# Kernel tuning notes

Measured on AMD Instinct MI355X. Metric: run time of the kernel, lower is better.

## Reference

```python
import jax, jax.numpy as jnp
import numpy as np

PATCH = 8          # patch_size
KEEP_RATIO = 0.7   # keep_ratio at full pruning progress (epoch >= 2*warmup)
MIN_PATCHES = 10


def setup_inputs() -> dict:
    key = jax.random.key(0)
    k_t, k_w1, k_w2 = jax.random.split(key, 3)
    B, H, W, C = 16, 128, 128, 256
    hidden = C // 4
    tokens = jax.random.normal(k_t, (B, H * W, C), dtype=jnp.float32)
    W1 = jax.random.normal(k_w1, (C, hidden), dtype=jnp.float32) * (1.0 / np.sqrt(C))
    b1 = jnp.zeros((hidden,), dtype=jnp.float32)
    W2 = jax.random.normal(k_w2, (hidden, 1), dtype=jnp.float32) * (1.0 / np.sqrt(hidden))
    b2 = jnp.zeros((1,), dtype=jnp.float32)
    return {"tokens": tokens, "W1": W1, "b1": b1, "W2": W2, "b2": b2, "H": H, "W": W}


def reference(tokens, W1, b1, W2, b2, H, W):
    B, N, C = tokens.shape
    ph = pw = PATCH
    nh, nw = H // ph, W // pw              # patches per dim (H,W divisible by PATCH)
    nP = nh * nw

    # ---- unfold into patches: [B, nP, ph*pw, C] (matches torch unfold layout) ----
    x = tokens.reshape(B, nh, ph, nw, pw, C)
    patches_flat = x.transpose(0, 1, 3, 2, 4, 5).reshape(B, nP, ph * pw, C)

    # ---- per-token importance (learnable MLP scorer), mean over patch tokens ----
    h = jax.nn.relu(jnp.einsum('bptc,cd->bptd', patches_flat, W1) + b1)
    tok_imp = jax.nn.sigmoid(jnp.einsum('bptd,do->bpto', h, W2) + b2)[..., 0]  # [B,nP,ph*pw]
    scores = tok_imp.mean(axis=-1)                                             # [B,nP]

    # ---- top-k patch selection, sorted ascending (keeps spatial order) ----
    nK = max(MIN_PATCHES, int(nP * KEEP_RATIO))  # 179 for 256 patches
    _, top_idx = jax.lax.top_k(scores, nK)
    top_idx = jnp.sort(top_idx, axis=-1)         # [B,nK]

    # ---- gather kept patches: [B, nK, ph, pw, C] ----
    patches = patches_flat.reshape(B, nP, ph, pw, C)
    kept = jnp.take_along_axis(patches, top_idx[:, :, None, None, None], axis=1)

    # ---- pad with zero patches to a full nKh x nKw grid, re-assemble 2D map ----
    nKh = -(-nK // nw)            # ceil
    nKw = min(nK, nw)
    pad = nKh * nKw - nK
    kept = jnp.pad(kept, ((0, 0), (0, pad), (0, 0), (0, 0), (0, 0)))
    out2d = kept.reshape(B, nKh, nKw, ph, pw, C).transpose(0, 1, 3, 2, 4, 5)
    H_new, W_new = nKh * ph, nKw * pw
    pruned_tokens = out2d.reshape(B, H_new * W_new, C)
    return pruned_tokens
```

## Files before the change

### kernel.cpp

```cpp
#include <hip/hip_runtime.h>
#include <math.h>

#define CCH   256
#define HID   64
#define MT    256
#define KC    32
#define XT    258
#define NP    256
#define NK    179
#define NSLOT 192
#define IMW   128
#define OUTH  96

typedef float f32x4 __attribute__((ext_vector_type(4)));

__global__ __launch_bounds__(256) void scorer_kernel(
    const float* __restrict__ tokens, const float* __restrict__ W1,
    const float* __restrict__ b1, const float* __restrict__ W2,
    const float* __restrict__ b2v, float* __restrict__ tok_imp)
{
    __shared__ float xs[KC * XT];
    __shared__ float ws[KC * HID];
    __shared__ float red[8 * MT];

    const int t  = threadIdx.x;
    const int tw = t & 31;
    const int hg = t >> 5;
    const long base = (long)blockIdx.x * MT;

    float w2r[8];
    float acc[8][8];
    #pragma unroll
    for (int j = 0; j < 8; ++j) w2r[j] = W2[hg * 8 + j];
    {
        float binit[8];
        #pragma unroll
        for (int j = 0; j < 8; ++j) binit[j] = b1[hg * 8 + j];
        #pragma unroll
        for (int i = 0; i < 8; ++i)
            #pragma unroll
            for (int j = 0; j < 8; ++j) acc[i][j] = binit[j];
    }

    const float4* tok4 = (const float4*)(tokens + base * CCH);
    const int f4k = t & 7;
    const int tl0 = t >> 3;

    float4 pf[8];
    #pragma unroll
    for (int pass = 0; pass < 8; ++pass)
        pf[pass] = tok4[(long)(tl0 + 32 * pass) * (CCH / 4) + f4k];
    float4 wpf0 = ((const float4*)W1)[t];
    float4 wpf1 = ((const float4*)W1)[t + 256];

    for (int ch = 0; ch < CCH / KC; ++ch) {
        #pragma unroll
        for (int pass = 0; pass < 8; ++pass) {
            int tokLocal = tl0 + 32 * pass;
            float4 v = pf[pass];
            int kloc = f4k * 4;
            xs[(kloc + 0) * XT + tokLocal] = v.x;
            xs[(kloc + 1) * XT + tokLocal] = v.y;
            xs[(kloc + 2) * XT + tokLocal] = v.z;
            xs[(kloc + 3) * XT + tokLocal] = v.w;
        }
        ((float4*)ws)[t]       = wpf0;
        ((float4*)ws)[t + 256] = wpf1;
        __syncthreads();

        if (ch < CCH / KC - 1) {
            #pragma unroll
            for (int pass = 0; pass < 8; ++pass)
                pf[pass] = tok4[(long)(tl0 + 32 * pass) * (CCH / 4)
                                + (ch + 1) * (KC / 4) + f4k];
            const float4* w14 = (const float4*)(W1 + (ch + 1) * KC * HID);
            wpf0 = w14[t];
            wpf1 = w14[t + 256];
        }

        #pragma unroll
        for (int kk = 0; kk < KC; ++kk) {
            float xv[8], wv[8];
            #pragma unroll
            for (int g = 0; g < 4; ++g) {
                xv[2 * g]     = xs[kk * XT + g * 64 + 2 * tw];
                xv[2 * g + 1] = xs[kk * XT + g * 64 + 2 * tw + 1];
            }
            #pragma unroll
            for (int j = 0; j < 8; ++j) wv[j] = ws[kk * HID + hg * 8 + j];
            #pragma unroll
            for (int i = 0; i < 8; ++i)
                #pragma unroll
                for (int j = 0; j < 8; ++j)
                    acc[i][j] = fmaf(xv[i], wv[j], acc[i][j]);
        }
        __syncthreads();
    }

    #pragma unroll
    for (int i = 0; i < 8; ++i) {
        float p = 0.f;
        #pragma unroll
        for (int j = 0; j < 8; ++j) {
            float h = acc[i][j] > 0.f ? acc[i][j] : 0.f;
            p = fmaf(h, w2r[j], p);
        }
        int g  = i >> 1;
        int lt = g * 64 + 2 * tw + (i & 1);
        red[hg * MT + lt] = p;
    }
    __syncthreads();
    float s = b2v[0];
    #pragma unroll
    for (int g = 0; g < 8; ++g) s += red[g * MT + t];
    tok_imp[base + t] = 1.f / (1.f + expf(-s));
}

__global__ __launch_bounds__(256) void select_kernel(
    const float* __restrict__ tok_imp, int* __restrict__ sel)
{
    __shared__ float s[NP];
    __shared__ unsigned long long wmask[4];
    const int b = blockIdx.x, p = threadIdx.x;
    const int ih = p >> 4, iw = p & 15;
    const float4* tp4 = (const float4*)(tok_imp + (long)b * 16384
                                        + (ih * 8) * IMW + iw * 8);
    float sum = 0.f;
    #pragma unroll
    for (int ti = 0; ti < 8; ++ti) {
        float4 a = tp4[ti * (IMW / 4)];
        float4 c = tp4[ti * (IMW / 4) + 1];
        sum += a.x; sum += a.y; sum += a.z; sum += a.w;
        sum += c.x; sum += c.y; sum += c.z; sum += c.w;
    }
    s[p] = sum;
    __syncthreads();
    const float sp = s[p];
    int rank = 0;
    #pragma unroll 8
    for (int j = 0; j < NP; ++j) {
        float sj = s[j];
        rank += (sj > sp) || ((sj == sp) && (j < p));
    }
    const bool keep = rank < NK;
    const unsigned long long m = __ballot(keep);
    const int wv = p >> 6, ln = p & 63;
    if (ln == 0) wmask[wv] = m;
    __syncthreads();
    if (keep) {
        int pos = __popcll(m & ((1ull << ln) - 1ull));
        #pragma unroll
        for (int w = 0; w < 3; ++w)
            if (w < wv) pos += __popcll(wmask[w]);
        sel[b * NK + pos] = p;
    }
}

__global__ __launch_bounds__(256) void gather_kernel(
    const float* __restrict__ tokens, const int* __restrict__ sel,
    float* __restrict__ out)
{
    const int bid = blockIdx.x;
    const int b = bid / NSLOT, k = bid % NSLOT;
    const int t = threadIdx.x;
    const int kh = k >> 4, kw = k & 15;
    f32x4* dst4 = (f32x4*)(out + (long)b * OUTH * IMW * CCH);

    if (k >= NK) {
        const f32x4 z = {0.f, 0.f, 0.f, 0.f};
        #pragma unroll
        for (int i = 0; i < 16; ++i) {
            int f = i * 256 + t;
            int ti = f >> 9;
            int off = f & 511;
            long d = ((long)(kh * 8 + ti) * IMW + kw * 8) * (CCH / 4) + off;
            __builtin_nontemporal_store(z, &dst4[d]);
        }
        return;
    }
    const int p = sel[b * NK + k];
    const int ih = p >> 4, iw = p & 15;
    const f32x4* src4 = (const f32x4*)(tokens + (long)b * 16384 * CCH);
    #pragma unroll
    for (int i = 0; i < 16; ++i) {
        int f = i * 256 + t;
        int ti = f >> 9;
        int off = f & 511;
        long srow = ((long)(ih * 8 + ti) * IMW + iw * 8) * (CCH / 4) + off;
        long drow = ((long)(kh * 8 + ti) * IMW + kw * 8) * (CCH / 4) + off;
        f32x4 v = src4[srow];
        __builtin_nontemporal_store(v, &dst4[drow]);
    }
}

extern "C" void kernel_launch(void* const* d_in, const int* in_sizes, int n_in,
                              void* d_out, int out_size, void* d_ws, size_t ws_size,
                              hipStream_t stream)
{
    const float* tokens = (const float*)d_in[0];
    const float* W1     = (const float*)d_in[1];
    const float* b1     = (const float*)d_in[2];
    const float* W2     = (const float*)d_in[3];
    const float* b2     = (const float*)d_in[4];

    const int totalTok = in_sizes[0] / CCH;
    const int B        = totalTok / (IMW * IMW);

    int*   sel     = (int*)d_ws;
    float* tok_imp;
    size_t selBytes = (size_t)B * NK * sizeof(int);
    size_t impBytes = (size_t)totalTok * sizeof(float);
    if (ws_size >= selBytes + 256 + impBytes) {
        tok_imp = (float*)((char*)d_ws + ((selBytes + 255) & ~(size_t)255));
    } else {
        tok_imp = (float*)d_out;
    }

    scorer_kernel<<<totalTok / MT, 256, 0, stream>>>(tokens, W1, b1, W2, b2, tok_imp);
    select_kernel<<<B, 256, 0, stream>>>(tok_imp, sel);
    gather_kernel<<<B * NSLOT, 256, 0, stream>>>(tokens, sel, (float*)d_out);
}
```

Measured before the change: 482.7 us.

## Remap scorer tile so each wave owns 16 hidden units with wave-uniform W1 loads

Reassigns the scorer GEMM so each wavefront covers 16 hidden columns and each lane 4 consecutive tokens. W1 is read directly from global memory through a wave-uniform (readfirstlane) pointer, which lets the compiler use scalar loads, so the W1 shared-memory staging is dropped. Token values are read from LDS as one float4 per k, with the row pitch padded to 260. This cuts LDS traffic and the ws buffer but puts scalar memory loads inside the inner loop, which may add latency.

```diff
diff --git a/kernel.cpp b/kernel.cpp
--- a/kernel.cpp
+++ b/kernel.cpp
@@ -5,7 +5,7 @@
 #define HID   64
 #define MT    256
 #define KC    32
-#define XT    258
+#define XT    260
 #define NP    256
 #define NK    179
 #define NSLOT 192
@@ -20,26 +20,26 @@
     const float* __restrict__ b2v, float* __restrict__ tok_imp)
 {
     __shared__ float xs[KC * XT];
-    __shared__ float ws[KC * HID];
     __shared__ float red[8 * MT];
 
-    const int t  = threadIdx.x;
-    const int tw = t & 31;
-    const int hg = t >> 5;
+    const int t    = threadIdx.x;
+    const int lane = t & 63;
+    const int wv   = t >> 6;
+    const int h0u  = __builtin_amdgcn_readfirstlane(wv * 16);
     const long base = (long)blockIdx.x * MT;
 
-    float w2r[8];
-    float acc[8][8];
-    #pragma unroll
-    for (int j = 0; j < 8; ++j) w2r[j] = W2[hg * 8 + j];
-    {
-        float binit[8];
-        #pragma unroll
-        for (int j = 0; j < 8; ++j) binit[j] = b1[hg * 8 + j];
-        #pragma unroll
-        for (int i = 0; i < 8; ++i)
-            #pragma unroll
-            for (int j = 0; j < 8; ++j) acc[i][j] = binit[j];
+    const float* __restrict__ w1u = W1 + h0u;
+
+    float w2r[16];
+    #pragma unroll
+    for (int j = 0; j < 16; ++j) w2r[j] = W2[h0u + j];
+
+    float acc[4][16];
+    #pragma unroll
+    for (int j = 0; j < 16; ++j) {
+        float bj = b1[h0u + j];
+        #pragma unroll
+        for (int i = 0; i < 4; ++i) acc[i][j] = bj;
     }
 
     const float4* tok4 = (const float4*)(tokens + base * CCH);
@@ -50,8 +50,6 @@
     #pragma unroll
     for (int pass = 0; pass < 8; ++pass)
         pf[pass] = tok4[(long)(tl0 + 32 * pass) * (CCH / 4) + f4k];
-    float4 wpf0 = ((const float4*)W1)[t];
-    float4 wpf1 = ((const float4*)W1)[t + 256];
 
     for (int ch = 0; ch < CCH / KC; ++ch) {
         #pragma unroll
@@ -64,8 +62,6 @@
             xs[(kloc + 2) * XT + tokLocal] = v.z;
             xs[(kloc + 3) * XT + tokLocal] = v.w;
         }
-        ((float4*)ws)[t]       = wpf0;
-        ((float4*)ws)[t + 256] = wpf1;
         __syncthreads();
 
         if (ch < CCH / KC - 1) {
@@ -73,41 +69,42 @@
             for (int pass = 0; pass < 8; ++pass)
                 pf[pass] = tok4[(long)(tl0 + 32 * pass) * (CCH / 4)
                                 + (ch + 1) * (KC / 4) + f4k];
-            const float4* w14 = (const float4*)(W1 + (ch + 1) * KC * HID);
-            wpf0 = w14[t];
-            wpf1 = w14[t + 256];
-        }
-
+        }
+
+        const float* __restrict__ wch = w1u + ch * KC * HID;
         #pragma unroll
         for (int kk = 0; kk < KC; ++kk) {
-            float xv[8], wv[8];
+            float4 xv = *(const float4*)&xs[kk * XT + 4 * lane];
+            float wr[16];
             #pragma unroll
-            for (int g = 0; g < 4; ++g) {
-                xv[2 * g]     = xs[kk * XT + g * 64 + 2 * tw];
-                xv[2 * g + 1] = xs[kk * XT + g * 64 + 2 * tw + 1];
+            for (int j = 0; j < 16; ++j) wr[j] = wch[kk * HID + j];
+            #pragma unroll
+            for (int j = 0; j < 16; ++j) {
+                acc[0][j] = fmaf(xv.x, wr[j], acc[0][j]);
+                acc[1][j] = fmaf(xv.y, wr[j], acc[1][j]);
+                acc[2][j] = fmaf(xv.z, wr[j], acc[2][j]);
+                acc[3][j] = fmaf(xv.w, wr[j], acc[3][j]);
             }
-            #pragma unroll
-            for (int j = 0; j < 8; ++j) wv[j] = ws[kk * HID + hg * 8 + j];
-            #pragma unroll
-            for (int i = 0; i < 8; ++i)
-                #pragma unroll
-                for (int j = 0; j < 8; ++j)
-                    acc[i][j] = fmaf(xv[i], wv[j], acc[i][j]);
         }
         __syncthreads();
     }
 
     #pragma unroll
-    for (int i = 0; i < 8; ++i) {
-        float p = 0.f;
+    for (int i = 0; i < 4; ++i) {
+        float p0 = 0.f, p1 = 0.f;
         #pragma unroll
         for (int j = 0; j < 8; ++j) {
             float h = acc[i][j] > 0.f ? acc[i][j] : 0.f;
-            p = fmaf(h, w2r[j], p);
-        }
-        int g  = i >> 1;
-        int lt = g * 64 + 2 * tw + (i & 1);
-        red[hg * MT + lt] = p;
+            p0 = fmaf(h, w2r[j], p0);
+        }
+        #pragma unroll
+        for (int j = 8; j < 16; ++j) {
+            float h = acc[i][j] > 0.f ? acc[i][j] : 0.f;
+            p1 = fmaf(h, w2r[j], p1);
+        }
+        int tok = lane * 4 + i;
+        red[(2 * wv) * MT + tok]     = p0;
+        red[(2 * wv + 1) * MT + tok] = p1;
     }
     __syncthreads();
     float s = b2v[0];
@@ -144,14 +141,14 @@
     }
     const bool keep = rank < NK;
     const unsigned long long m = __ballot(keep);
-    const int wv = p >> 6, ln = p & 63;
-    if (ln == 0) wmask[wv] = m;
+    const int wvi = p >> 6, ln = p & 63;
+    if (ln == 0) wmask[wvi] = m;
     __syncthreads();
     if (keep) {
         int pos = __popcll(m & ((1ull << ln) - 1ull));
         #pragma unroll
         for (int w = 0; w < 3; ++w)
-            if (w < wv) pos += __popcll(wmask[w]);
+            if (w < wvi) pos += __popcll(wmask[w]);
         sel[b * NK + pos] = p;
     }
 }
```

New measurement: 562.8 us. +16.6%, slower.
